# Kernel tuning notes

Measured on AMD Instinct MI355X. Metric: run time of the kernel, lower is better.

Reference implementation:

```python
import jax, jax.numpy as jnp
import numpy as np
import math

EMBED_DIM = 1024
NUM_HEADS = 16
HEAD_DIM = EMBED_DIM // NUM_HEADS
B, S = 2, 2048


def setup_inputs() -> dict:
    key = jax.random.key(0)
    ks = jax.random.split(key, 13)
    sc = 1.0 / math.sqrt(EMBED_DIM)
    inp = {
        "query": jax.random.normal(ks[0], (B, S, EMBED_DIM), jnp.float32),
        "key": jax.random.normal(ks[1], (B, S, EMBED_DIM), jnp.float32),
        "value": jax.random.normal(ks[2], (B, S, EMBED_DIM), jnp.float32),
        "input_patch_mask": jax.random.randint(ks[3], (B, S), 0, 2, jnp.int32),
        "Wq": jax.random.normal(ks[4], (EMBED_DIM, EMBED_DIM), jnp.float32) * sc,
        "bq": jnp.zeros((EMBED_DIM,), jnp.float32),
        "Wk": jax.random.normal(ks[5], (EMBED_DIM, EMBED_DIM), jnp.float32) * sc,
        "bk": jnp.zeros((EMBED_DIM,), jnp.float32),
        "Wv": jax.random.normal(ks[6], (EMBED_DIM, EMBED_DIM), jnp.float32) * sc,
        "bv": jnp.zeros((EMBED_DIM,), jnp.float32),
        "Wo": jax.random.normal(ks[7], (EMBED_DIM, EMBED_DIM), jnp.float32) * sc,
        "bo": jnp.zeros((EMBED_DIM,), jnp.float32),
    }
    return inp


def _masked_softmax(scores, mask):
    # Equivalent to masked_fill(-inf) -> softmax -> nan_to_num(0.0):
    # fully-masked rows produce exactly 0, without generating NaNs.
    neg_inf = jnp.array(-jnp.inf, scores.dtype)
    s = jnp.where(mask, scores, neg_inf)
    m = jnp.max(s, axis=-1, keepdims=True)
    m_safe = jnp.where(jnp.isfinite(m), m, jnp.zeros_like(m))
    e = jnp.where(mask, jnp.exp(s - m_safe), 0.0)
    denom = jnp.sum(e, axis=-1, keepdims=True)
    denom = jnp.where(denom == 0.0, 1.0, denom)
    return e / denom


def reference(query, key, value, input_patch_mask, Wq, bq, Wk, bk, Wv, bv, Wo, bo):
    b, s, d = query.shape
    h, hd = NUM_HEADS, HEAD_DIM
    q = (query @ Wq.T + bq).reshape(b, s, h, hd).transpose(0, 2, 1, 3)  # [b,h,s,hd]
    k = (key @ Wk.T + bk).reshape(b, s, h, hd).transpose(0, 2, 1, 3)
    v = (value @ Wv.T + bv).reshape(b, s, h, hd).transpose(0, 2, 1, 3)
    scores = jnp.einsum("bhqd,bhkd->bhqk", q, k) / math.sqrt(hd)
    # mask[b,i,j] = patch_mask[b,i] * patch_mask[b,j]
    mask = (input_patch_mask[:, :, None] * input_patch_mask[:, None, :]) > 0
    attn = _masked_softmax(scores, mask[:, None, :, :])  # dropout in eval mode = identity
    context = jnp.einsum("bhqk,bhkd->bhqd", attn, v)
    context = context.transpose(0, 2, 1, 3).reshape(b, s, d)
    return context @ Wo.T + bo
```

## Files before the change

kernel.cpp:

```cpp
#include <hip/hip_runtime.h>
#include <cstdint>
#include <cstddef>

#define EMBED 1024
#define NHEAD 16
#define HD    64
#define BATCH 2
#define SEQ   2048
#define MROWS (BATCH*SEQ)
#define QSCALE 0.1803368801111137f

typedef __bf16 bf16;
typedef __bf16 bf16x8 __attribute__((ext_vector_type(8)));
typedef float  f32x4  __attribute__((ext_vector_type(4)));
typedef unsigned int u32;

#if __has_builtin(__builtin_amdgcn_exp2f)
#define EXP2(x) __builtin_amdgcn_exp2f(x)
#else
#define EXP2(x) exp2f(x)
#endif

typedef const u32 __attribute__((address_space(1)))* gp_t;
typedef u32 __attribute__((address_space(3)))* lp_t;

__device__ __forceinline__ void g2l16(const void* g, void* l) {
  __builtin_amdgcn_global_load_lds((gp_t)(uintptr_t)g, (lp_t)(u32)(uintptr_t)l, 16, 0, 0);
}

#define MFMA(a, b, c) __builtin_amdgcn_mfma_f32_16x16x32_bf16((a), (b), (c), 0, 0, 0)

__global__ void cast_multi(const float* __restrict__ p0, const float* __restrict__ p1,
                           const float* __restrict__ p2, const float* __restrict__ p3,
                           bf16* o0, bf16* o1, bf16* o2, bf16* o3, int n8) {
  int z = blockIdx.y;
  const float* in = z==0?p0 : z==1?p1 : z==2?p2 : p3;
  bf16*       out = z==0?o0 : z==1?o1 : z==2?o2 : o3;
  int i = blockIdx.x * blockDim.x + threadIdx.x;
  if (i >= n8) return;
  const float4* p = (const float4*)in;
  float4 a = p[2*i], b = p[2*i+1];
  union { bf16 h[8]; uint4 u; } r;
  r.h[0] = (bf16)a.x; r.h[1] = (bf16)a.y; r.h[2] = (bf16)a.z; r.h[3] = (bf16)a.w;
  r.h[4] = (bf16)b.x; r.h[5] = (bf16)b.y; r.h[6] = (bf16)b.z; r.h[7] = (bf16)b.w;
  ((uint4*)out)[i] = r.u;
}

#define BM 128
#define BN 128
#define BK 32
#define NKI (EMBED/BK)

__device__ __forceinline__ void gemm_core(
    const bf16* __restrict__ A, const bf16* __restrict__ W,
    bf16* Al, bf16* Bl, f32x4 (&acc)[4][4])
{
  const int tid  = threadIdx.x;
  const int lane = tid & 63, wid = tid >> 6;
  const int quad = lane >> 4, l16 = lane & 15;
  const int wm = wid >> 1, wn = wid & 1;
  const int m0 = blockIdx.y * BM, n0 = blockIdx.x * BN;

  const int R = tid >> 2, Cc = tid & 3;
  const int gcol = (Cc ^ ((R >> 1) & 3)) * 8;
  const bf16* Ag = A + (size_t)(m0 + R) * EMBED + gcol;
  const bf16* Bg = W + (size_t)(n0 + R) * EMBED + gcol;
  bf16* AlW = Al + wid * 512;
  bf16* BlW = Bl + wid * 512;

  g2l16(Ag, AlW);                      g2l16(Ag + (size_t)64*EMBED, AlW + 2048);
  g2l16(Bg, BlW);                      g2l16(Bg + (size_t)64*EMBED, BlW + 2048);
  __syncthreads();

  for (int ki = 0; ki < NKI; ++ki) {
    const int cur = ki & 1;
    if (ki + 1 < NKI) {
      const int nb = cur ^ 1;
      const int k0 = (ki + 1) * BK;
      g2l16(Ag + k0, AlW + nb*4096);
      g2l16(Ag + (size_t)64*EMBED + k0, AlW + nb*4096 + 2048);
      g2l16(Bg + k0, BlW + nb*4096);
      g2l16(Bg + (size_t)64*EMBED + k0, BlW + nb*4096 + 2048);
    }
    const bf16* Ac = Al + cur*4096;
    const bf16* Bc = Bl + cur*4096;
    bf16x8 af[4], bg[4];
#pragma unroll
    for (int i = 0; i < 4; ++i) {
      int ra = wm*64 + i*16 + l16;
      af[i] = *(const bf16x8*)(Ac + ra*32 + ((quad ^ ((ra>>1)&3))*8));
      int rb = wn*64 + i*16 + l16;
      bg[i] = *(const bf16x8*)(Bc + rb*32 + ((quad ^ ((rb>>1)&3))*8));
    }
#pragma unroll
    for (int i = 0; i < 4; ++i)
#pragma unroll
      for (int j = 0; j < 4; ++j)
        acc[i][j] = MFMA(af[i], bg[j], acc[i][j]);
    __syncthreads();
  }
}

__global__ __launch_bounds__(256) void qkv_kernel(
    const bf16* __restrict__ Xq, const bf16* __restrict__ Xk, const bf16* __restrict__ Xv,
    const bf16* __restrict__ Wq, const bf16* __restrict__ Wk, const bf16* __restrict__ Wv,
    const float* __restrict__ bq, const float* __restrict__ bk, const float* __restrict__ bv,
    bf16* __restrict__ Qp, bf16* __restrict__ Kp, bf16* __restrict__ VTg)
{
  __shared__ bf16 Al[2*BM*BK];
  __shared__ bf16 Bl[2*BN*BK];
  const int z = blockIdx.z;
  const bf16* A = z==0 ? Xq : z==1 ? Xk : Xv;
  const bf16* W = z==0 ? Wq : z==1 ? Wk : Wv;
  const float* bias = z==0 ? bq : z==1 ? bk : bv;
  const float scale = (z==0) ? QSCALE : 1.0f;

  f32x4 acc[4][4] = {};
  gemm_core(A, W, Al, Bl, acc);

  const int lane = threadIdx.x & 63, wid = threadIdx.x >> 6;
  const int quad = lane >> 4, l16 = lane & 15;
  const int wm = wid >> 1, wn = wid & 1;
  const int m0 = blockIdx.y * BM, n0 = blockIdx.x * BN;

#pragma unroll
  for (int i = 0; i < 4; ++i) {
#pragma unroll
    for (int j = 0; j < 4; ++j) {
      int col = n0 + wn*64 + j*16 + l16;
      float bv2 = bias[col];
      if (z < 2) {
        bf16* outp = (z == 0) ? Qp : Kp;
#pragma unroll
        for (int r = 0; r < 4; ++r) {
          int row = m0 + wm*64 + i*16 + quad*4 + r;
          outp[(size_t)row*EMBED + col] = (bf16)((acc[i][j][r] + bv2) * scale);
        }
      } else {
        int row0 = m0 + wm*64 + i*16 + quad*4;
        int bb = row0 >> 11, ss = row0 & (SEQ-1);
        int hh = col >> 6, dd = col & (HD-1);
        union { bf16 h4[4]; uint2 u; } pk;
#pragma unroll
        for (int r = 0; r < 4; ++r) pk.h4[r] = (bf16)(acc[i][j][r] + bv2);
        *(uint2*)(VTg + (((size_t)bb*NHEAD + hh)*HD + dd)*SEQ + ss) = pk.u;
      }
    }
  }
}

__global__ __launch_bounds__(256) void oproj_kernel(
    const bf16* __restrict__ Ctx, const bf16* __restrict__ Wo,
    const float* __restrict__ bo, float* __restrict__ out)
{
  __shared__ bf16 Al[2*BM*BK];
  __shared__ bf16 Bl[2*BN*BK];
  f32x4 acc[4][4] = {};
  gemm_core(Ctx, Wo, Al, Bl, acc);

  const int lane = threadIdx.x & 63, wid = threadIdx.x >> 6;
  const int quad = lane >> 4, l16 = lane & 15;
  const int wm = wid >> 1, wn = wid & 1;
  const int m0 = blockIdx.y * BM, n0 = blockIdx.x * BN;
#pragma unroll
  for (int i = 0; i < 4; ++i)
#pragma unroll
    for (int j = 0; j < 4; ++j) {
      int col = n0 + wn*64 + j*16 + l16;
      float bv = bo[col];
#pragma unroll
      for (int r = 0; r < 4; ++r) {
        int row = m0 + wm*64 + i*16 + quad*4 + r;
        out[(size_t)row*EMBED + col] = (acc[i][j][r] + bv);
      }
    }
}

#define NT  (SEQ/64)
#define PST 72

__global__ __launch_bounds__(256, 3) void attn_kernel(
    const bf16* __restrict__ Qp, const bf16* __restrict__ Kp, const bf16* __restrict__ VT,
    const int* __restrict__ pmask, bf16* __restrict__ Ctx)
{
  __shared__ bf16 Kt[2][64*64];
  __shared__ bf16 Vt[2][64*64];
  __shared__ bf16 Pl[4][16*PST];

  const int qt = blockIdx.x, h = blockIdx.y, b = blockIdx.z;
  const int tid = threadIdx.x, lane = tid & 63, wid = tid >> 6;
  const int quad = lane >> 4, l16 = lane & 15;
  const int qrow0 = qt*64 + wid*16;

  const size_t qoff = (size_t)(b*SEQ + qrow0 + l16)*EMBED + h*HD;
  bf16x8 qf0 = *(const bf16x8*)(Qp + qoff + quad*8);
  bf16x8 qf1 = *(const bf16x8*)(Qp + qoff + 32 + quad*8);

  int qm[4];
#pragma unroll
  for (int r = 0; r < 4; ++r) qm[r] = pmask[b*SEQ + qrow0 + quad*4 + r];

  bf16 onev = (bf16)1.0f;
  bf16x8 ones = {onev, onev, onev, onev, onev, onev, onev, onev};

  const bf16* Kg  = Kp + (size_t)b*SEQ*EMBED + h*HD;
  const bf16* VTg = VT + (size_t)(b*NHEAD + h)*HD*SEQ;

  const int R = tid >> 3;
  const int Cc = tid & 7;
  const int scol = (Cc ^ (R & 7)) * 8;

  f32x4 o[4] = {};
  f32x4 lacc = {};

#define STAGE(kt, buf) do {                                              \
    const bf16* kg = Kg + (size_t)((kt)*64 + R)*EMBED + scol;            \
    const bf16* vg = VTg + (size_t)R*SEQ + (kt)*64 + scol;               \
    bf16* kl = &Kt[buf][0] + wid*512;                                    \
    bf16* vl = &Vt[buf][0] + wid*512;                                    \
    g2l16(kg, kl);  g2l16(kg + (size_t)32*EMBED, kl + 2048);             \
    g2l16(vg, vl);  g2l16(vg + (size_t)32*SEQ,   vl + 2048);             \
  } while (0)

  STAGE(0, 0);
  __syncthreads();

  for (int kt = 0; kt < NT; ++kt) {
    const int cur = kt & 1;
    if (kt + 1 < NT) STAGE(kt + 1, cur ^ 1);
    const bf16* Kc = &Kt[cur][0];
    const bf16* Vc = &Vt[cur][0];

#pragma unroll
    for (int g = 0; g < 4; ++g) {
      int ra = g*16 + l16, sa = ra & 7;
      bf16x8 kfa = *(const bf16x8*)(Kc + ra*64 + ((quad     ^ sa)*8));
      bf16x8 kfb = *(const bf16x8*)(Kc + ra*64 + (((quad+4) ^ sa)*8));
      f32x4 sg = {};
      sg = MFMA(qf0, kfa, sg);
      sg = MFMA(qf1, kfb, sg);
      int km = pmask[b*SEQ + kt*64 + g*16 + l16];
#pragma unroll
      for (int r = 0; r < 4; ++r) {
        float sv = km ? sg[r] : -__builtin_inff();
        Pl[wid][(quad*4 + r)*PST + g*16 + l16] = (bf16)EXP2(sv);
      }
    }

    bf16x8 pf0 = *(const bf16x8*)(&Pl[wid][l16*PST + quad*8]);
    bf16x8 pf1 = *(const bf16x8*)(&Pl[wid][l16*PST + 32 + quad*8]);
    lacc = MFMA(pf0, ones, lacc);
    lacc = MFMA(pf1, ones, lacc);
#pragma unroll
    for (int t = 0; t < 4; ++t) {
      int rd = t*16 + l16, sd = rd & 7;
      bf16x8 vf0 = *(const bf16x8*)(Vc + rd*64 + ((quad     ^ sd)*8));
      bf16x8 vf1 = *(const bf16x8*)(Vc + rd*64 + (((quad+4) ^ sd)*8));
      o[t] = MFMA(pf0, vf0, o[t]);
      o[t] = MFMA(pf1, vf1, o[t]);
    }
    __syncthreads();
  }

  float inv[4];
#pragma unroll
  for (int r = 0; r < 4; ++r)
    inv[r] = (qm[r] && lacc[r] > 0.f) ? 1.0f / lacc[r] : 0.0f;

#pragma unroll
  for (int t = 0; t < 4; ++t)
#pragma unroll
    for (int r = 0; r < 4; ++r) {
      int row = b*SEQ + qrow0 + quad*4 + r;
      Ctx[(size_t)row*EMBED + h*HD + t*16 + l16] = (bf16)(o[t][r] * inv[r]);
    }
}

extern "C" void kernel_launch(void* const* d_in, const int* in_sizes, int n_in,
                              void* d_out, int out_size, void* d_ws, size_t ws_size,
                              hipStream_t stream)
{
  const float* query = (const float*)d_in[0];
  const float* key   = (const float*)d_in[1];
  const float* value = (const float*)d_in[2];
  const int*   pm    = (const int*)d_in[3];
  const float* Wq = (const float*)d_in[4];
  const float* bq = (const float*)d_in[5];
  const float* Wk = (const float*)d_in[6];
  const float* bk = (const float*)d_in[7];
  const float* Wv = (const float*)d_in[8];
  const float* bv = (const float*)d_in[9];
  const float* Wo = (const float*)d_in[10];
  const float* bo = (const float*)d_in[11];
  float* out = (float*)d_out;

  const size_t SZ_X = (size_t)MROWS * EMBED;
  const size_t SZ_W = (size_t)EMBED * EMBED;

  bf16* p   = (bf16*)d_ws;
  bf16* Xq  = p; p += SZ_X;
  bf16* Xk  = p; p += SZ_X;
  bf16* Xv  = p; p += SZ_X;
  bf16* Wqb = p; p += SZ_W;
  bf16* Wkb = p; p += SZ_W;
  bf16* Wvb = p; p += SZ_W;
  bf16* Wob = p; p += SZ_W;
  bf16* Qp  = p; p += SZ_X;
  bf16* Kp  = p; p += SZ_X;
  bf16* VTg = p; p += SZ_X;
  bf16* Ctx = p; p += SZ_X;

  dim3 gx((unsigned)(SZ_X/8/256), 3);
  cast_multi<<<gx, 256, 0, stream>>>(query, key, value, query, Xq, Xk, Xv, Xq, (int)(SZ_X/8));
  dim3 gw((unsigned)(SZ_W/8/256), 4);
  cast_multi<<<gw, 256, 0, stream>>>(Wq, Wk, Wv, Wo, Wqb, Wkb, Wvb, Wob, (int)(SZ_W/8));

  dim3 gq(EMBED/BN, MROWS/BM, 3);
  qkv_kernel<<<gq, 256, 0, stream>>>(Xq, Xk, Xv, Wqb, Wkb, Wvb, bq, bk, bv, Qp, Kp, VTg);

  dim3 ga(SEQ/64, NHEAD, BATCH);
  attn_kernel<<<ga, 256, 0, stream>>>(Qp, Kp, VTg, pm, Ctx);

  dim3 gg(EMBED/BN, MROWS/BM);
  oproj_kernel<<<gg, 256, 0, stream>>>(Ctx, Wob, bo, out);
}
```

Before: 256.0 us.

## Double query rows per attention wave and use smaller output-projection tiles

The attention kernel now has each wave process 32 query rows instead of 16. Every K/V tile staged in shared memory is therefore reused across twice as many queries, and the grid along the sequence is halved. The output projection drops the shared gemm_core for a dedicated 128x64 tile kernel with its own double buffering, which doubles the block count for better CU coverage. The costs are more registers per attention wave, which threatens the 3-blocks-per-CU occupancy target, and fewer attention blocks overall.

```diff
diff --git a/kernel.cpp b/kernel.cpp
--- a/kernel.cpp
+++ b/kernel.cpp
@@ -153,31 +153,71 @@
     const bf16* __restrict__ Ctx, const bf16* __restrict__ Wo,
     const float* __restrict__ bo, float* __restrict__ out)
 {
-  __shared__ bf16 Al[2*BM*BK];
-  __shared__ bf16 Bl[2*BN*BK];
-  f32x4 acc[4][4] = {};
-  gemm_core(Ctx, Wo, Al, Bl, acc);
-
-  const int lane = threadIdx.x & 63, wid = threadIdx.x >> 6;
+  __shared__ bf16 Al[2*128*32];
+  __shared__ bf16 Bl[2*64*32];
+  const int tid  = threadIdx.x;
+  const int lane = tid & 63, wid = tid >> 6;
   const int quad = lane >> 4, l16 = lane & 15;
-  const int wm = wid >> 1, wn = wid & 1;
-  const int m0 = blockIdx.y * BM, n0 = blockIdx.x * BN;
-#pragma unroll
-  for (int i = 0; i < 4; ++i)
+  const int m0 = blockIdx.y * 128, n0 = blockIdx.x * 64;
+
+  const int R = tid >> 2, Cc = tid & 3;
+  const int gcol = (Cc ^ ((R >> 1) & 3)) * 8;
+  const bf16* Ag = Ctx + (size_t)(m0 + R) * EMBED + gcol;
+  const bf16* Bg = Wo  + (size_t)(n0 + R) * EMBED + gcol;
+  bf16* AlW = Al + wid * 512;
+  bf16* BlW = Bl + wid * 512;
+
+  g2l16(Ag, AlW);  g2l16(Ag + (size_t)64*EMBED, AlW + 2048);
+  g2l16(Bg, BlW);
+  __syncthreads();
+
+  f32x4 acc[2][4] = {};
+  for (int ki = 0; ki < NKI; ++ki) {
+    const int cur = ki & 1;
+    if (ki + 1 < NKI) {
+      const int nb = cur ^ 1;
+      const int k0 = (ki + 1) * BK;
+      g2l16(Ag + k0, AlW + nb*4096);
+      g2l16(Ag + (size_t)64*EMBED + k0, AlW + nb*4096 + 2048);
+      g2l16(Bg + k0, BlW + nb*2048);
+    }
+    const bf16* Ac = Al + cur*4096;
+    const bf16* Bc = Bl + cur*2048;
+    bf16x8 af[2], bg[4];
+#pragma unroll
+    for (int u = 0; u < 2; ++u) {
+      int ra = wid*32 + u*16 + l16;
+      af[u] = *(const bf16x8*)(Ac + ra*32 + ((quad ^ ((ra>>1)&3))*8));
+    }
 #pragma unroll
     for (int j = 0; j < 4; ++j) {
-      int col = n0 + wn*64 + j*16 + l16;
+      int rb = j*16 + l16;
+      bg[j] = *(const bf16x8*)(Bc + rb*32 + ((quad ^ ((rb>>1)&3))*8));
+    }
+#pragma unroll
+    for (int u = 0; u < 2; ++u)
+#pragma unroll
+      for (int j = 0; j < 4; ++j)
+        acc[u][j] = MFMA(af[u], bg[j], acc[u][j]);
+    __syncthreads();
+  }
+
+#pragma unroll
+  for (int u = 0; u < 2; ++u)
+#pragma unroll
+    for (int j = 0; j < 4; ++j) {
+      int col = n0 + j*16 + l16;
       float bv = bo[col];
 #pragma unroll
       for (int r = 0; r < 4; ++r) {
-        int row = m0 + wm*64 + i*16 + quad*4 + r;
-        out[(size_t)row*EMBED + col] = (acc[i][j][r] + bv);
+        int row = m0 + wid*32 + u*16 + quad*4 + r;
+        out[(size_t)row*EMBED + col] = (acc[u][j][r] + bv);
       }
     }
 }
 
 #define NT  (SEQ/64)
-#define PST 72
+#define PST 68
 
 __global__ __launch_bounds__(256, 3) void attn_kernel(
     const bf16* __restrict__ Qp, const bf16* __restrict__ Kp, const bf16* __restrict__ VT,
@@ -185,20 +225,26 @@
 {
   __shared__ bf16 Kt[2][64*64];
   __shared__ bf16 Vt[2][64*64];
-  __shared__ bf16 Pl[4][16*PST];
+  __shared__ bf16 Pl[4][32*PST];
 
   const int qt = blockIdx.x, h = blockIdx.y, b = blockIdx.z;
   const int tid = threadIdx.x, lane = tid & 63, wid = tid >> 6;
   const int quad = lane >> 4, l16 = lane & 15;
-  const int qrow0 = qt*64 + wid*16;
-
-  const size_t qoff = (size_t)(b*SEQ + qrow0 + l16)*EMBED + h*HD;
-  bf16x8 qf0 = *(const bf16x8*)(Qp + qoff + quad*8);
-  bf16x8 qf1 = *(const bf16x8*)(Qp + qoff + 32 + quad*8);
-
-  int qm[4];
-#pragma unroll
-  for (int r = 0; r < 4; ++r) qm[r] = pmask[b*SEQ + qrow0 + quad*4 + r];
+  const int qrow0 = qt*128 + wid*32;
+
+  bf16x8 qf[2][2];
+#pragma unroll
+  for (int u = 0; u < 2; ++u) {
+    const size_t qoff = (size_t)(b*SEQ + qrow0 + u*16 + l16)*EMBED + h*HD;
+    qf[u][0] = *(const bf16x8*)(Qp + qoff + quad*8);
+    qf[u][1] = *(const bf16x8*)(Qp + qoff + 32 + quad*8);
+  }
+
+  int qm[2][4];
+#pragma unroll
+  for (int u = 0; u < 2; ++u)
+#pragma unroll
+    for (int r = 0; r < 4; ++r) qm[u][r] = pmask[b*SEQ + qrow0 + u*16 + quad*4 + r];
 
   bf16 onev = (bf16)1.0f;
   bf16x8 ones = {onev, onev, onev, onev, onev, onev, onev, onev};
@@ -210,8 +256,8 @@
   const int Cc = tid & 7;
   const int scol = (Cc ^ (R & 7)) * 8;
 
-  f32x4 o[4] = {};
-  f32x4 lacc = {};
+  f32x4 o[2][4] = {};
+  f32x4 lacc[2] = {};
 
 #define STAGE(kt, buf) do {                                              \
     const bf16* kg = Kg + (size_t)((kt)*64 + R)*EMBED + scol;            \
@@ -236,44 +282,56 @@
       int ra = g*16 + l16, sa = ra & 7;
       bf16x8 kfa = *(const bf16x8*)(Kc + ra*64 + ((quad     ^ sa)*8));
       bf16x8 kfb = *(const bf16x8*)(Kc + ra*64 + (((quad+4) ^ sa)*8));
-      f32x4 sg = {};
-      sg = MFMA(qf0, kfa, sg);
-      sg = MFMA(qf1, kfb, sg);
       int km = pmask[b*SEQ + kt*64 + g*16 + l16];
 #pragma unroll
-      for (int r = 0; r < 4; ++r) {
-        float sv = km ? sg[r] : -__builtin_inff();
-        Pl[wid][(quad*4 + r)*PST + g*16 + l16] = (bf16)EXP2(sv);
-      }
-    }
-
-    bf16x8 pf0 = *(const bf16x8*)(&Pl[wid][l16*PST + quad*8]);
-    bf16x8 pf1 = *(const bf16x8*)(&Pl[wid][l16*PST + 32 + quad*8]);
-    lacc = MFMA(pf0, ones, lacc);
-    lacc = MFMA(pf1, ones, lacc);
+      for (int u = 0; u < 2; ++u) {
+        f32x4 sg = {};
+        sg = MFMA(qf[u][0], kfa, sg);
+        sg = MFMA(qf[u][1], kfb, sg);
+#pragma unroll
+        for (int r = 0; r < 4; ++r) {
+          float pv = km ? EXP2(sg[r]) : 0.0f;
+          Pl[wid][(u*16 + quad*4 + r)*PST + g*16 + l16] = (bf16)pv;
+        }
+      }
+    }
+
+    bf16x8 pf[2][2];
+#pragma unroll
+    for (int u = 0; u < 2; ++u) {
+      pf[u][0] = *(const bf16x8*)(&Pl[wid][(u*16 + l16)*PST + quad*8]);
+      pf[u][1] = *(const bf16x8*)(&Pl[wid][(u*16 + l16)*PST + 32 + quad*8]);
+      lacc[u] = MFMA(pf[u][0], ones, lacc[u]);
+      lacc[u] = MFMA(pf[u][1], ones, lacc[u]);
+    }
 #pragma unroll
     for (int t = 0; t < 4; ++t) {
       int rd = t*16 + l16, sd = rd & 7;
       bf16x8 vf0 = *(const bf16x8*)(Vc + rd*64 + ((quad     ^ sd)*8));
       bf16x8 vf1 = *(const bf16x8*)(Vc + rd*64 + (((quad+4) ^ sd)*8));
-      o[t] = MFMA(pf0, vf0, o[t]);
-      o[t] = MFMA(pf1, vf1, o[t]);
+#pragma unroll
+      for (int u = 0; u < 2; ++u) {
+        o[u][t] = MFMA(pf[u][0], vf0, o[u][t]);
+        o[u][t] = MFMA(pf[u][1], vf1, o[u][t]);
+      }
     }
     __syncthreads();
   }
 
-  float inv[4];
-#pragma unroll
-  for (int r = 0; r < 4; ++r)
-    inv[r] = (qm[r] && lacc[r] > 0.f) ? 1.0f / lacc[r] : 0.0f;
-
-#pragma unroll
-  for (int t = 0; t < 4; ++t)
-#pragma unroll
-    for (int r = 0; r < 4; ++r) {
-      int row = b*SEQ + qrow0 + quad*4 + r;
-      Ctx[(size_t)row*EMBED + h*HD + t*16 + l16] = (bf16)(o[t][r] * inv[r]);
-    }
+#pragma unroll
+  for (int u = 0; u < 2; ++u) {
+    float inv[4];
+#pragma unroll
+    for (int r = 0; r < 4; ++r)
+      inv[r] = (qm[u][r] && lacc[u][r] > 0.f) ? 1.0f / lacc[u][r] : 0.0f;
+#pragma unroll
+    for (int t = 0; t < 4; ++t)
+#pragma unroll
+      for (int r = 0; r < 4; ++r) {
+        int row = b*SEQ + qrow0 + u*16 + quad*4 + r;
+        Ctx[(size_t)row*EMBED + h*HD + t*16 + l16] = (bf16)(o[u][t][r] * inv[r]);
+      }
+  }
 }
 
 extern "C" void kernel_launch(void* const* d_in, const int* in_sizes, int n_in,
@@ -318,9 +376,9 @@
   dim3 gq(EMBED/BN, MROWS/BM, 3);
   qkv_kernel<<<gq, 256, 0, stream>>>(Xq, Xk, Xv, Wqb, Wkb, Wvb, bq, bk, bv, Qp, Kp, VTg);
 
-  dim3 ga(SEQ/64, NHEAD, BATCH);
+  dim3 ga(SEQ/128, NHEAD, BATCH);
   attn_kernel<<<ga, 256, 0, stream>>>(Qp, Kp, VTg, pm, Ctx);
 
-  dim3 gg(EMBED/BN, MROWS/BM);
+  dim3 gg(EMBED/64, MROWS/128);
   oproj_kernel<<<gg, 256, 0, stream>>>(Ctx, Wob, bo, out);
 }
```

Result: faster. 237.3 us (-7.3%).
